# Performance work log

Hardware: AMD Instinct MI355X
Metric: run time of the kernel (lower is better)

The kernel has to match this reference:

```python
import jax, jax.numpy as jnp
import numpy as np

DIM, HEADS, DEPTH, SEQ, LOCAL_W = 1024, 16, 7, 2048, 64
HEAD_DIM = DIM // HEADS
SCALE = 1.0 / HEAD_DIM ** 0.5


def cantor_mask(S, depth, local_window):
    """Allowed (i,j): |i-j| within local window, OR |i-j| lies in the Cantor set
    under `depth` levels of ternary subdivision (no base-3 digit equals 1)."""
    idx = np.arange(S)
    d = np.abs(idx[:, None] - idx[None, :])
    x = d.copy()
    ok = np.ones_like(d, dtype=bool)
    for _ in range(depth):
        ok &= (x % 3) != 1
        x //= 3
    ok &= x == 0  # offset must be < 3**depth
    return jnp.asarray(ok | (d <= local_window))  # [S, S] bool


def setup_inputs() -> dict:
    key = jax.random.key(0)
    ks = jax.random.split(key, 8)
    B = 2
    s = 0.02
    return {
        "query": jax.random.normal(ks[0], (B, SEQ, DIM), jnp.float32),
        "key_value": jax.random.normal(ks[1], (B, SEQ, DIM), jnp.float32),
        "Wq": jax.random.normal(ks[2], (DIM, DIM), jnp.float32) * s,
        "bq": jnp.zeros((DIM,), jnp.float32),
        "Wkv": jax.random.normal(ks[3], (DIM, 2 * DIM), jnp.float32) * s,
        "bkv": jnp.zeros((2 * DIM,), jnp.float32),
        "Wo": jax.random.normal(ks[4], (DIM, DIM), jnp.float32) * s,
        "bo": jnp.zeros((DIM,), jnp.float32),
    }


def reference(query, key_value, Wq, bq, Wkv, bkv, Wo, bo):
    B, S, D = query.shape
    H, hd = HEADS, HEAD_DIM
    mask = cantor_mask(S, DEPTH, LOCAL_W)  # static [S, S] bool

    q = (query @ Wq + bq).reshape(B, S, H, hd).transpose(0, 2, 1, 3)  # [B,H,S,hd]
    kv = (key_value @ Wkv + bkv).reshape(B, S, 2, H, hd).transpose(2, 0, 3, 1, 4)
    k, v = kv[0], kv[1]  # [B,H,S,hd]

    scores = jnp.einsum("bhqd,bhkd->bhqk", q, k) * SCALE
    scores = jnp.where(mask, scores, jnp.finfo(scores.dtype).min)
    attn = jax.nn.softmax(scores, axis=-1)
    out = jnp.einsum("bhqk,bhkd->bhqd", attn, v)  # [B,H,S,hd]
    out = out.transpose(0, 2, 1, 3).reshape(B, S, D)
    return out @ Wo + bo
```

## Files before the change

kernel.cpp:

```cpp
#include <hip/hip_runtime.h>
#include <stdint.h>

typedef _Float16 half_t;
typedef __attribute__((ext_vector_type(8))) _Float16 half8;
typedef __attribute__((ext_vector_type(4))) _Float16 half4;
typedef __attribute__((ext_vector_type(4))) float floatx4;
typedef __attribute__((ext_vector_type(2))) uint32_t uint32x2;

#define SEQ 2048
#define NH 16
#define HD 64

#define MFMA16(a, b, c) __builtin_amdgcn_mfma_f32_16x16x16f16(a, b, c, 0, 0, 0)
#define MFMA32K(a, b, c) __builtin_amdgcn_mfma_f32_16x16x32_f16(a, b, c, 0, 0, 0)

#define QSCALE 0.1803368801111306f

__global__ __launch_bounds__(256) void prep(
    const float* __restrict__ query, const float* __restrict__ key_value,
    const float* __restrict__ Wq, const float* __restrict__ Wkv,
    const float* __restrict__ Wo, half_t* __restrict__ xq,
    half_t* __restrict__ xkv, half_t* __restrict__ wqT,
    half_t* __restrict__ wkvT, half_t* __restrict__ woT,
    uint8_t* __restrict__ tok, uint8_t* __restrict__ tok16,
    uint64_t* __restrict__ maskw) {
  int bx = blockIdx.x, tid = threadIdx.x;
  if (bx < 2048) {
    const float* s; half_t* d; int base;
    if (bx < 1024) { s = query; d = xq; base = bx * 4096; }
    else { s = key_value; d = xkv; base = (bx - 1024) * 4096; }
#pragma unroll
    for (int u = 0; u < 4; ++u) {
      int i = base + u * 1024 + tid * 4;
      floatx4 v = *(const floatx4*)(s + i);
      half4 h;
      h[0] = (half_t)v[0]; h[1] = (half_t)v[1];
      h[2] = (half_t)v[2]; h[3] = (half_t)v[3];
      *(half4*)(d + i) = h;
    }
    return;
  }
  if (bx < 4096) {
    __shared__ float tile[32][33];
    int tx = tid & 31, ty = tid >> 5;
    const int K = 1024;
#pragma unroll
    for (int u = 0; u < 2; ++u) {
      int t = (bx - 2048) * 2 + u;
      const float* W; half_t* Wt; int N, nt, kt;
      if (t < 1024) { W = Wq; Wt = wqT; N = 1024; nt = t & 31; kt = t >> 5; }
      else if (t < 3072) { int t2 = t - 1024; W = Wkv; Wt = wkvT; N = 2048; nt = t2 & 63; kt = t2 >> 6; }
      else { int t2 = t - 3072; W = Wo; Wt = woT; N = 1024; nt = t2 & 31; kt = t2 >> 5; }
      int n0 = nt * 32, k0 = kt * 32;
#pragma unroll
      for (int i = 0; i < 4; ++i)
        tile[ty + i * 8][tx] = W[(size_t)(k0 + ty + i * 8) * N + n0 + tx];
      __syncthreads();
#pragma unroll
      for (int i = 0; i < 4; ++i)
        Wt[(size_t)(n0 + ty + i * 8) * K + k0 + tx] = (half_t)tile[tx][ty + i * 8];
      __syncthreads();
    }
    return;
  }
  __shared__ uint8_t slut[2048];
  int ib = bx - 4096;
  for (int d = tid; d < 2048; d += 256) {
    int x = d;
    bool ok = true;
    for (int it = 0; it < 7; ++it) { ok &= ((x % 3) != 1); x /= 3; }
    ok &= (x == 0);
    slut[d] = (ok || d <= 64) ? 1 : 0;
  }
  __syncthreads();
  if (ib == 0) {
    if (tid < 64) {
      int delta = tid - 32;
      int lo = delta * 64 - 63, hi = delta * 64 + 63;
      uint8_t any = 0;
      for (int x = lo; x <= hi; ++x) {
        int a = x < 0 ? -x : x;
        if (a < 2048) any |= slut[a];
      }
      tok[tid] = any;
    }
    {
      int d16 = tid - 128;
      int ctr = d16 * 16;
      uint8_t any = 0;
      for (int x = ctr - 15; x <= ctr + 15; ++x) {
        int a = x < 0 ? -x : x;
        if (a < 2048) any |= slut[a];
      }
      tok16[tid] = any;
    }
  }
  int g = ib * 256 + tid;
  int tt = g - 2048;
  uint64_t w = 0;
  for (int jj = 0; jj < 64; ++jj) {
    int d = tt - jj; d = d < 0 ? -d : d;
    if (d < 2048 && slut[d]) w |= (1ull << jj);
  }
  maskw[g] = w;
}

__device__ __forceinline__ void cp16(half_t* lds, const half_t* g) {
  __builtin_amdgcn_global_load_lds(
      (const __attribute__((address_space(1))) uint32_t*)g,
      (__attribute__((address_space(3))) uint32_t*)lds, 16, 0, 0);
}

__global__ __launch_bounds__(256) void gemm_qkv(
    const half_t* __restrict__ xq, const half_t* __restrict__ xkv,
    const half_t* __restrict__ wqT, const half_t* __restrict__ wkvT,
    const float* __restrict__ bq, const float* __restrict__ bkv,
    half_t* __restrict__ qout, half_t* __restrict__ kout,
    half_t* __restrict__ vTout) {
  extern __shared__ char smemraw[];
  half_t* As = (half_t*)smemraw;
  half_t* Bs = As + 12288;
  const int K = 1024;
  bool isq = blockIdx.y < 8;
  const half_t* A = isq ? xq : xkv;
  const half_t* Bt = isq ? wqT : wkvT;
  const float* bias = isq ? bq : bkv;
  int n0 = (isq ? blockIdx.y : (blockIdx.y - 8)) * 128;
  int m0 = blockIdx.x * 128;

  int tid = threadIdx.x;
  int wave = tid >> 6, lane = tid & 63;
  int c = lane & 15, quad = lane >> 4;
  int wm = (wave >> 1) * 64, wn = (wave & 1) * 64;

  floatx4 acc[4][4] = {};
  int arow = tid >> 2;
  int akc = ((tid & 3) ^ (arow & 3)) * 8;
  int csw = c & 3;

#define QKV_ISSUE(kt2)                                                        \
  {                                                                           \
    int s_ = (kt2) % 3;                                                       \
    int k0_ = (kt2) * 32;                                                     \
    cp16(&As[s_ * 4096 + wave * 512], A + (size_t)(m0 + arow) * K + k0_ + akc);          \
    cp16(&As[s_ * 4096 + 2048 + wave * 512], A + (size_t)(m0 + 64 + arow) * K + k0_ + akc); \
    cp16(&Bs[s_ * 4096 + wave * 512], Bt + (size_t)(n0 + arow) * K + k0_ + akc);         \
    cp16(&Bs[s_ * 4096 + 2048 + wave * 512], Bt + (size_t)(n0 + 64 + arow) * K + k0_ + akc); \
  }

  QKV_ISSUE(0)
  QKV_ISSUE(1)

  for (int kt = 0; kt < 32; ++kt) {
    if (kt < 31) {
      asm volatile("s_waitcnt vmcnt(4)" ::: "memory");
    } else {
      asm volatile("s_waitcnt vmcnt(0)" ::: "memory");
    }
    __builtin_amdgcn_s_barrier();
    if (kt + 2 < 32) QKV_ISSUE(kt + 2)
    int b = kt % 3;
    half8 af[4], bf[4];
#pragma unroll
    for (int mt = 0; mt < 4; ++mt)
      af[mt] = *(const half8*)&As[b * 4096 + (wm + mt * 16 + c) * 32 + ((quad ^ csw) * 8)];
#pragma unroll
    for (int nt = 0; nt < 4; ++nt)
      bf[nt] = *(const half8*)&Bs[b * 4096 + (wn + nt * 16 + c) * 32 + ((quad ^ csw) * 8)];
#pragma unroll
    for (int mt = 0; mt < 4; ++mt)
#pragma unroll
      for (int nt = 0; nt < 4; ++nt)
        acc[mt][nt] = MFMA32K(af[mt], bf[nt], acc[mt][nt]);
  }
#undef QKV_ISSUE

  __syncthreads();
  half_t* ep = (half_t*)smemraw;
  int bb = m0 >> 11, sbase = m0 & 2047;
  bool isv = (!isq) && (n0 >= 1024);

  if (!isv) {
#pragma unroll
    for (int nt = 0; nt < 4; ++nt) {
      int nl = wn + nt * 16 + c;
      float bv = bias[n0 + nl];
#pragma unroll
      for (int mt = 0; mt < 4; ++mt)
#pragma unroll
        for (int r = 0; r < 4; ++r) {
          int ml = wm + mt * 16 + quad * 4 + r;
          float v = acc[mt][nt][r] + bv;
          if (isq) v *= QSCALE;
          ep[ml * 132 + nl] = (half_t)v;
        }
    }
    __syncthreads();
    half_t* outp = isq ? qout : kout;
#pragma unroll
    for (int rd = 0; rd < 8; ++rd) {
      int id = rd * 256 + tid;
      int ml = id >> 4, ch = id & 15;
      int ng = n0 + ch * 8;
      int h = ng >> 6, d0 = ng & 63;
      half8 v = *(const half8*)&ep[ml * 132 + ch * 8];
      *(half8*)(outp + ((size_t)(bb * 16 + h) * SEQ + sbase + ml) * 64 + d0) = v;
    }
  } else {
#pragma unroll
    for (int nt = 0; nt < 4; ++nt) {
      int nl = wn + nt * 16 + c;
      float bv = bias[n0 + nl];
#pragma unroll
      for (int mt = 0; mt < 4; ++mt) {
        int ml = wm + mt * 16 + quad * 4;
        half4 hv;
#pragma unroll
        for (int r = 0; r < 4; ++r) hv[r] = (half_t)(acc[mt][nt][r] + bv);
        *(half4*)&ep[nl * 136 + ml] = hv;
      }
    }
    __syncthreads();
#pragma unroll
    for (int rd = 0; rd < 8; ++rd) {
      int id = rd * 256 + tid;
      int nl = id >> 4, mc = id & 15;
      int ng = n0 + nl;
      int h = (ng >> 6) & 15, d = ng & 63;
      half8 v = *(const half8*)&ep[nl * 136 + mc * 8];
      *(half8*)(vTout + ((size_t)(bb * 16 + h) * 64 + d) * SEQ + sbase + mc * 8) = v;
    }
  }
}

__global__ __launch_bounds__(256) void gemm_out(
    const half_t* __restrict__ A, const half_t* __restrict__ Bt,
    const float* __restrict__ bias, float* __restrict__ outf) {
  __shared__ half_t As[3][128 * 32];
  __shared__ half_t Bs[3][64 * 32];
  const int K = 1024;
  int tid = threadIdx.x;
  int wave = tid >> 6, lane = tid & 63;
  int c = lane & 15, quad = lane >> 4;
  int wm = (wave >> 1) * 64, wn = (wave & 1) * 32;
  int m0 = blockIdx.x * 128, n0 = blockIdx.y * 64;

  floatx4 acc[4][2] = {};
  int arow = tid >> 2;
  int akc = ((tid & 3) ^ (arow & 3)) * 8;
  int csw = c & 3;

#define OUT_ISSUE(kt2)                                                        \
  {                                                                           \
    int s_ = (kt2) % 3;                                                       \
    int k0_ = (kt2) * 32;                                                     \
    cp16(&As[s_][wave * 512], A + (size_t)(m0 + arow) * K + k0_ + akc);       \
    cp16(&As[s_][2048 + wave * 512], A + (size_t)(m0 + 64 + arow) * K + k0_ + akc); \
    cp16(&Bs[s_][wave * 512], Bt + (size_t)(n0 + arow) * K + k0_ + akc);      \
  }

  OUT_ISSUE(0)
  OUT_ISSUE(1)

  for (int kt = 0; kt < 32; ++kt) {
    if (kt < 31) {
      asm volatile("s_waitcnt vmcnt(3)" ::: "memory");
    } else {
      asm volatile("s_waitcnt vmcnt(0)" ::: "memory");
    }
    __builtin_amdgcn_s_barrier();
    if (kt + 2 < 32) OUT_ISSUE(kt + 2)
    int b = kt % 3;
    half8 af[4], bf[2];
#pragma unroll
    for (int mt = 0; mt < 4; ++mt)
      af[mt] = *(const half8*)&As[b][(wm + mt * 16 + c) * 32 + ((quad ^ csw) * 8)];
#pragma unroll
    for (int nt = 0; nt < 2; ++nt)
      bf[nt] = *(const half8*)&Bs[b][(wn + nt * 16 + c) * 32 + ((quad ^ csw) * 8)];
#pragma unroll
    for (int mt = 0; mt < 4; ++mt)
#pragma unroll
      for (int nt = 0; nt < 2; ++nt)
        acc[mt][nt] = MFMA32K(af[mt], bf[nt], acc[mt][nt]);
  }
#undef OUT_ISSUE

#pragma unroll
  for (int nt = 0; nt < 2; ++nt) {
    int n = n0 + wn + nt * 16 + c;
    float bv = bias[n];
#pragma unroll
    for (int mt = 0; mt < 4; ++mt)
#pragma unroll
      for (int r = 0; r < 4; ++r) {
        int m = m0 + wm + mt * 16 + quad * 4 + r;
        outf[(size_t)m * 1024 + n] = acc[mt][nt][r] + bv;
      }
  }
}

__global__ __launch_bounds__(512) void attn_kernel(
    const half_t* __restrict__ qb, const half_t* __restrict__ kb,
    const half_t* __restrict__ vTg, half_t* __restrict__ ctx,
    const uint64_t* __restrict__ maskw, const uint8_t* __restrict__ tok,
    const uint8_t* __restrict__ tok16g) {
  __shared__ half_t kT[64 * 64];
  __shared__ half_t vT[64 * 64];
  __shared__ half_t ot[128 * 72];
  __shared__ int list[34];
  __shared__ uint8_t tok16s[256];
  __shared__ uint32_t mlut[16][2];

  int tid = threadIdx.x, wave = tid >> 6, lane = tid & 63;
  int c = lane & 15, q = lane >> 4;
  int id = blockIdx.x;
  int bh = (id & 7) * 4 + ((id >> 3) & 3);
  int it128 = id >> 5;
  int i0 = it128 << 7;
  const half_t* qbase = qb + (size_t)bh * SEQ * HD;
  const half_t* kg = kb + (size_t)bh * SEQ * HD;
  const half_t* vg = vTg + (size_t)bh * HD * SEQ;

  if (tid < 256) tok16s[tid] = tok16g[tid];
  if (tid >= 256 && tid < 272) {
    int t = tid - 256;
    mlut[t][0] = (t & 1 ? 0xFFFFu : 0u) | (t & 2 ? 0xFFFF0000u : 0u);
    mlut[t][1] = (t & 4 ? 0xFFFFu : 0u) | (t & 8 ? 0xFFFF0000u : 0u);
  }
  if (wave == 0) {
    int jt = lane;
    int base = i0 >> 6;
    bool act = (jt < 32) &&
               (tok[(jt - base) + 32] | tok[(jt - base - 1) + 32]);
    unsigned long long bal = __ballot(act);
    if (act) {
      int pre = __popcll(bal & ((1ull << jt) - 1));
      list[1 + pre] = jt << 6;
    }
    if (lane == 0) list[0] = __popcll(bal);
  }

  int i_row = i0 + wave * 16 + c;
  int it16 = (i0 >> 4) + wave;
  half8 qf0 = *(const half8*)(qbase + (size_t)i_row * 64 + q * 8);
  half8 qf1 = *(const half8*)(qbase + (size_t)i_row * 64 + 32 + q * 8);

  floatx4 oacc[4] = {};
  floatx4 lacc = {};
  half4 ones;
  ones[0] = (half_t)1.f; ones[1] = (half_t)1.f;
  ones[2] = (half_t)1.f; ones[3] = (half_t)1.f;

  int srow = tid >> 3;
  int sch = tid & 7;
  int ssw = srow & 7;

  __syncthreads();
  int nact = list[0];
  int j0 = list[1];

  half8 kr = *(const half8*)(kg + (size_t)(j0 + srow) * 64 + sch * 8);
  half8 vr = *(const half8*)(vg + (size_t)srow * SEQ + j0 + sch * 8);
  uint64_t wcur = maskw[(i_row - j0) + 2048];

  for (int ti = 0; ti < nact; ++ti) {
    int bidx = (j0 >> 4) - it16 + 128;
    __syncthreads();
    *(half8*)&kT[srow * 64 + ((sch ^ ssw) * 8)] = kr;
    *(half8*)&vT[srow * 64 + ((sch ^ ssw) * 8)] = vr;
    int j0n = (ti + 1 < nact) ? list[2 + ti] : j0;
    __syncthreads();

    uint64_t wnext = wcur;
    if (ti + 1 < nact) {
      kr = *(const half8*)(kg + (size_t)(j0n + srow) * 64 + sch * 8);
      vr = *(const half8*)(vg + (size_t)srow * SEQ + j0n + sch * 8);
      wnext = maskw[(i_row - j0n) + 2048];
    }

    uint32_t wlo = (uint32_t)(wcur >> (4 * q));
    uint32_t whi = (uint32_t)(wcur >> (32 + 4 * q));
    uint32x2 mm[4];
#pragma unroll
    for (int jt = 0; jt < 4; ++jt) {
      uint32_t ww = (jt < 2) ? wlo : whi;
      uint32_t nib = (ww >> (16 * (jt & 1))) & 15u;
      mm[jt] = *(const uint32x2*)&mlut[nib][0];
    }
#pragma unroll
    for (int jt = 0; jt < 4; ++jt) {
      if (!tok16s[bidx + jt]) continue;
      int row = jt * 16 + c;
      int sw = c & 7;
      half8 a0 = *(const half8*)&kT[row * 64 + ((q ^ sw) * 8)];
      half8 a1 = *(const half8*)&kT[row * 64 + (((4 + q) ^ sw) * 8)];
      floatx4 t = {};
      t = MFMA32K(a0, qf0, t);
      t = MFMA32K(a1, qf1, t);
      float p0 = __builtin_exp2f(t[0]);
      float p1 = __builtin_exp2f(t[1]);
      float p2 = __builtin_exp2f(t[2]);
      float p3 = __builtin_exp2f(t[3]);
      auto lo = __builtin_amdgcn_cvt_pkrtz(p0, p1);
      auto hi = __builtin_amdgcn_cvt_pkrtz(p2, p3);
      union { uint32_t u[2]; half4 h4; } pu;
      pu.u[0] = __builtin_bit_cast(uint32_t, lo) & mm[jt][0];
      pu.u[1] = __builtin_bit_cast(uint32_t, hi) & mm[jt][1];
      half4 pb = pu.h4;
      lacc = MFMA16(ones, pb, lacc);
#pragma unroll
      for (int mt = 0; mt < 4; ++mt) {
        int drow = mt * 16 + c;
        int ch = 2 * jt + (q >> 1);
        half4 a = *(const half4*)&vT[drow * 64 + ((ch ^ sw) * 8) + (q & 1) * 4];
        oacc[mt] = MFMA16(a, pb, oacc[mt]);
      }
    }
    wcur = wnext;
    j0 = j0n;
  }

  float inv_l = 1.0f / lacc[0];
#pragma unroll
  for (int mt = 0; mt < 4; ++mt)
#pragma unroll
    for (int r = 0; r < 4; ++r)
      ot[(wave * 16 + c) * 72 + mt * 16 + 4 * q + r] = (half_t)(oacc[mt][r] * inv_l);
  __syncthreads();
  {
    int row = tid >> 2, chq = tid & 3;
    int b = bh >> 4, h = bh & 15;
    size_t base = (((size_t)(b * SEQ + i0 + row) * NH) + h) * 64 + chq * 16;
    half8 v0 = *(const half8*)&ot[row * 72 + chq * 16];
    half8 v1 = *(const half8*)&ot[row * 72 + chq * 16 + 8];
    *(half8*)(ctx + base) = v0;
    *(half8*)(ctx + base + 8) = v1;
  }
}

extern "C" void kernel_launch(void* const* d_in, const int* in_sizes, int n_in,
                              void* d_out, int out_size, void* d_ws, size_t ws_size,
                              hipStream_t stream) {
  const float* query = (const float*)d_in[0];
  const float* key_value = (const float*)d_in[1];
  const float* Wq = (const float*)d_in[2];
  const float* bq = (const float*)d_in[3];
  const float* Wkv = (const float*)d_in[4];
  const float* bkv = (const float*)d_in[5];
  const float* Wo = (const float*)d_in[6];
  const float* bo = (const float*)d_in[7];

  char* ws = (char*)d_ws;
  uint8_t* tok = (uint8_t*)ws;
  uint8_t* tok16 = (uint8_t*)(ws + 1024);
  uint64_t* maskw = (uint64_t*)(ws + 4096);
  const size_t MB = 1ull << 20;
  half_t* xq = (half_t*)(ws + 1 * MB);
  half_t* xkv = (half_t*)(ws + 9 * MB);
  half_t* wqT = (half_t*)(ws + 17 * MB);
  half_t* wkvT = (half_t*)(ws + 19 * MB);
  half_t* woT = (half_t*)(ws + 23 * MB);
  half_t* qbuf = (half_t*)(ws + 25 * MB);
  half_t* kbuf = (half_t*)(ws + 33 * MB);
  half_t* vTg = (half_t*)(ws + 41 * MB);
  half_t* ctx = xq;

  hipLaunchKernelGGL(prep, dim3(4112), dim3(256), 0, stream,
                     query, key_value, Wq, Wkv, Wo, xq, xkv, wqT, wkvT, woT,
                     tok, tok16, maskw);
  hipLaunchKernelGGL(gemm_qkv, dim3(32, 24), dim3(256), 49152, stream,
                     xq, xkv, wqT, wkvT, bq, bkv, qbuf, kbuf, vTg);
  hipLaunchKernelGGL(attn_kernel, dim3(512), dim3(512), 0, stream,
                     qbuf, kbuf, vTg, ctx, maskw, tok, tok16);
  hipLaunchKernelGGL(gemm_out, dim3(32, 16), dim3(256), 0, stream,
                     ctx, woT, bo, (float*)d_out);
}
```

Before: 210.6 us.

## Enlarge QKV GEMM to 256x256 tiles with 8 waves and phased pipelining

Rewrites the QKV projection GEMM to use 256x256 output tiles per 512-thread block with K-step 64 and double-buffered LDS of 128KB. The main loop is split into four quadrant phases, each overlapping the async global-to-LDS loads for the next K tile with MFMA work, using sched_barrier and setprio. The aim is to raise arithmetic intensity and hide load latency better than the earlier 128x128 triple-buffered loop. The trade-off is only 192 blocks on the grid with one block per CU, so fill of the wave-level work may drop, and register pressure rises from the larger accumulator set.

New measurement: 220.0 us. 1.04x slower.

```diff
diff --git a/kernel.cpp b/kernel.cpp
--- a/kernel.cpp
+++ b/kernel.cpp
@@ -111,7 +111,53 @@
       (__attribute__((address_space(3))) uint32_t*)lds, 16, 0, 0);
 }
 
-__global__ __launch_bounds__(256) void gemm_qkv(
+#define VMC(n) asm volatile("s_waitcnt vmcnt(" #n ")" ::: "memory")
+
+#define STG_A(kt2, mh)                                                        \
+  {                                                                           \
+    half_t* d_ = &As[(((kt2) & 1) * 2 + (mh)) * 8192 + wave * 512];           \
+    const half_t* s_ = A + (size_t)(m0 + (mh) * 128 + r1) * K + (kt2) * 64 + hsw; \
+    cp16(d_, s_);                                                             \
+    cp16(d_ + 4096, s_ + (size_t)64 * K);                                     \
+  }
+#define STG_B(kt2, nh)                                                        \
+  {                                                                           \
+    half_t* d_ = &Bs[(((kt2) & 1) * 2 + (nh)) * 8192 + wave * 512];           \
+    const half_t* s_ = Bt + (size_t)(n0 + (nh) * 128 + r1) * K + (kt2) * 64 + hsw; \
+    cp16(d_, s_);                                                             \
+    cp16(d_ + 4096, s_ + (size_t)64 * K);                                     \
+  }
+
+#define PHASE(KB, MQ, NQ, ...)                                                \
+  do {                                                                        \
+    __builtin_amdgcn_s_barrier();                                             \
+    __builtin_amdgcn_sched_barrier(0);                                        \
+    const half_t* Ab = &As[((KB) * 2 + (MQ)) * 8192];                         \
+    const half_t* Bb = &Bs[((KB) * 2 + (NQ)) * 8192];                         \
+    half8 af[4][2], bf[2][2];                                                 \
+    _Pragma("unroll") for (int i_ = 0; i_ < 4; ++i_) {                        \
+      int rl_ = mw * 64 + i_ * 16 + c;                                        \
+      af[i_][0] = *(const half8*)&Ab[rl_ * 64 + ((quad * 8) ^ rsw)];          \
+      af[i_][1] = *(const half8*)&Ab[rl_ * 64 + ((32 + quad * 8) ^ rsw)];     \
+    }                                                                         \
+    _Pragma("unroll") for (int j_ = 0; j_ < 2; ++j_) {                        \
+      int cl_ = nw * 32 + j_ * 16 + c;                                        \
+      bf[j_][0] = *(const half8*)&Bb[cl_ * 64 + ((quad * 8) ^ rsw)];          \
+      bf[j_][1] = *(const half8*)&Bb[cl_ * 64 + ((32 + quad * 8) ^ rsw)];     \
+    }                                                                         \
+    __VA_ARGS__;                                                              \
+    __builtin_amdgcn_sched_barrier(0);                                        \
+    __builtin_amdgcn_s_barrier();                                             \
+    __builtin_amdgcn_s_setprio(1);                                            \
+    _Pragma("unroll") for (int i_ = 0; i_ < 4; ++i_)                          \
+      _Pragma("unroll") for (int j_ = 0; j_ < 2; ++j_) {                      \
+        acc[MQ][NQ][i_][j_] = MFMA32K(af[i_][0], bf[j_][0], acc[MQ][NQ][i_][j_]); \
+        acc[MQ][NQ][i_][j_] = MFMA32K(af[i_][1], bf[j_][1], acc[MQ][NQ][i_][j_]); \
+      }                                                                       \
+    __builtin_amdgcn_s_setprio(0);                                            \
+  } while (0)
+
+__global__ __launch_bounds__(512, 1) void gemm_qkv(
     const half_t* __restrict__ xq, const half_t* __restrict__ xkv,
     const half_t* __restrict__ wqT, const half_t* __restrict__ wkvT,
     const float* __restrict__ bq, const float* __restrict__ bkv,
@@ -119,61 +165,43 @@
     half_t* __restrict__ vTout) {
   extern __shared__ char smemraw[];
   half_t* As = (half_t*)smemraw;
-  half_t* Bs = As + 12288;
-  const int K = 1024;
-  bool isq = blockIdx.y < 8;
+  half_t* Bs = As + 32768;
+  const int K = 1024, NT = 16;
+  bool isq = blockIdx.y < 4;
   const half_t* A = isq ? xq : xkv;
   const half_t* Bt = isq ? wqT : wkvT;
   const float* bias = isq ? bq : bkv;
-  int n0 = (isq ? blockIdx.y : (blockIdx.y - 8)) * 128;
-  int m0 = blockIdx.x * 128;
+  int n0 = (isq ? blockIdx.y : (blockIdx.y - 4)) * 256;
+  int m0 = blockIdx.x * 256;
 
   int tid = threadIdx.x;
   int wave = tid >> 6, lane = tid & 63;
   int c = lane & 15, quad = lane >> 4;
-  int wm = (wave >> 1) * 64, wn = (wave & 1) * 64;
-
-  floatx4 acc[4][4] = {};
-  int arow = tid >> 2;
-  int akc = ((tid & 3) ^ (arow & 3)) * 8;
-  int csw = c & 3;
-
-#define QKV_ISSUE(kt2)                                                        \
-  {                                                                           \
-    int s_ = (kt2) % 3;                                                       \
-    int k0_ = (kt2) * 32;                                                     \
-    cp16(&As[s_ * 4096 + wave * 512], A + (size_t)(m0 + arow) * K + k0_ + akc);          \
-    cp16(&As[s_ * 4096 + 2048 + wave * 512], A + (size_t)(m0 + 64 + arow) * K + k0_ + akc); \
-    cp16(&Bs[s_ * 4096 + wave * 512], Bt + (size_t)(n0 + arow) * K + k0_ + akc);         \
-    cp16(&Bs[s_ * 4096 + 2048 + wave * 512], Bt + (size_t)(n0 + 64 + arow) * K + k0_ + akc); \
-  }
-
-  QKV_ISSUE(0)
-  QKV_ISSUE(1)
-
-  for (int kt = 0; kt < 32; ++kt) {
-    if (kt < 31) {
-      asm volatile("s_waitcnt vmcnt(4)" ::: "memory");
-    } else {
-      asm volatile("s_waitcnt vmcnt(0)" ::: "memory");
-    }
-    __builtin_amdgcn_s_barrier();
-    if (kt + 2 < 32) QKV_ISSUE(kt + 2)
-    int b = kt % 3;
-    half8 af[4], bf[4];
-#pragma unroll
-    for (int mt = 0; mt < 4; ++mt)
-      af[mt] = *(const half8*)&As[b * 4096 + (wm + mt * 16 + c) * 32 + ((quad ^ csw) * 8)];
-#pragma unroll
-    for (int nt = 0; nt < 4; ++nt)
-      bf[nt] = *(const half8*)&Bs[b * 4096 + (wn + nt * 16 + c) * 32 + ((quad ^ csw) * 8)];
-#pragma unroll
-    for (int mt = 0; mt < 4; ++mt)
-#pragma unroll
-      for (int nt = 0; nt < 4; ++nt)
-        acc[mt][nt] = MFMA32K(af[mt], bf[nt], acc[mt][nt]);
-  }
-#undef QKV_ISSUE
+  int mw = wave >> 2, nw = wave & 3;
+
+  floatx4 acc[2][2][4][2] = {};
+
+  int r1 = tid >> 3;
+  int hh = (tid & 7) * 8;
+  int hsw = hh ^ (((r1 >> 2) & 1) << 4);
+  int rsw = ((c >> 2) & 1) << 4;
+
+  STG_A(0, 0); STG_B(0, 0); STG_B(0, 1); STG_A(0, 1);
+
+  for (int kt = 0; kt + 1 < NT; ++kt) {
+    int kb = kt & 1, kn = kt + 1;
+    VMC(4); PHASE(kb, 0, 0, STG_A(kn, 0));
+    VMC(4); PHASE(kb, 0, 1, STG_B(kn, 0));
+    VMC(4); PHASE(kb, 1, 0, STG_B(kn, 1));
+            PHASE(kb, 1, 1, STG_A(kn, 1));
+  }
+  {
+    int kb = (NT - 1) & 1;
+    VMC(4); PHASE(kb, 0, 0, (void)0);
+    VMC(2); PHASE(kb, 0, 1, (void)0);
+    VMC(0); PHASE(kb, 1, 0, (void)0);
+            PHASE(kb, 1, 1, (void)0);
+  }
 
   __syncthreads();
   half_t* ep = (half_t*)smemraw;
@@ -181,57 +209,71 @@
   bool isv = (!isq) && (n0 >= 1024);
 
   if (!isv) {
-#pragma unroll
-    for (int nt = 0; nt < 4; ++nt) {
-      int nl = wn + nt * 16 + c;
-      float bv = bias[n0 + nl];
-#pragma unroll
-      for (int mt = 0; mt < 4; ++mt)
-#pragma unroll
-        for (int r = 0; r < 4; ++r) {
-          int ml = wm + mt * 16 + quad * 4 + r;
-          float v = acc[mt][nt][r] + bv;
-          if (isq) v *= QSCALE;
-          ep[ml * 132 + nl] = (half_t)v;
-        }
-    }
-    __syncthreads();
     half_t* outp = isq ? qout : kout;
 #pragma unroll
-    for (int rd = 0; rd < 8; ++rd) {
-      int id = rd * 256 + tid;
-      int ml = id >> 4, ch = id & 15;
-      int ng = n0 + ch * 8;
-      int h = ng >> 6, d0 = ng & 63;
-      half8 v = *(const half8*)&ep[ml * 132 + ch * 8];
-      *(half8*)(outp + ((size_t)(bb * 16 + h) * SEQ + sbase + ml) * 64 + d0) = v;
+    for (int nq = 0; nq < 2; ++nq) {
+      if (nq) __syncthreads();
+#pragma unroll
+      for (int mq = 0; mq < 2; ++mq)
+#pragma unroll
+        for (int i = 0; i < 4; ++i)
+#pragma unroll
+          for (int j = 0; j < 2; ++j) {
+            int row = mq * 128 + mw * 64 + i * 16 + quad * 4;
+            int cl = nw * 32 + j * 16 + c;
+            float bv = bias[n0 + nq * 128 + cl];
+#pragma unroll
+            for (int r = 0; r < 4; ++r) {
+              float v = acc[mq][nq][i][j][r] + bv;
+              if (isq) v *= QSCALE;
+              ep[(row + r) * 132 + cl] = (half_t)v;
+            }
+          }
+      __syncthreads();
+#pragma unroll
+      for (int rd = 0; rd < 8; ++rd) {
+        int id = rd * 512 + tid;
+        int ml = id >> 4, ch = id & 15;
+        int ng = n0 + nq * 128 + ch * 8;
+        int h = ng >> 6, d0 = ng & 63;
+        half8 v = *(const half8*)&ep[ml * 132 + ch * 8];
+        *(half8*)(outp + ((size_t)(bb * 16 + h) * SEQ + sbase + ml) * 64 + d0) = v;
+      }
     }
   } else {
 #pragma unroll
-    for (int nt = 0; nt < 4; ++nt) {
-      int nl = wn + nt * 16 + c;
-      float bv = bias[n0 + nl];
-#pragma unroll
-      for (int mt = 0; mt < 4; ++mt) {
-        int ml = wm + mt * 16 + quad * 4;
-        half4 hv;
-#pragma unroll
-        for (int r = 0; r < 4; ++r) hv[r] = (half_t)(acc[mt][nt][r] + bv);
-        *(half4*)&ep[nl * 136 + ml] = hv;
+    for (int nq = 0; nq < 2; ++nq) {
+      if (nq) __syncthreads();
+#pragma unroll
+      for (int mq = 0; mq < 2; ++mq)
+#pragma unroll
+        for (int i = 0; i < 4; ++i)
+#pragma unroll
+          for (int j = 0; j < 2; ++j) {
+            int row = mq * 128 + mw * 64 + i * 16 + quad * 4;
+            int cl = nw * 32 + j * 16 + c;
+            float bv = bias[n0 + nq * 128 + cl];
+            half4 hv;
+#pragma unroll
+            for (int r = 0; r < 4; ++r) hv[r] = (half_t)(acc[mq][nq][i][j][r] + bv);
+            *(half4*)&ep[cl * 264 + row] = hv;
+          }
+      __syncthreads();
+#pragma unroll
+      for (int rd = 0; rd < 8; ++rd) {
+        int id = rd * 512 + tid;
+        int dl = id >> 5, mc = id & 31;
+        int ng = n0 + nq * 128 + dl;
+        int h = (ng >> 6) & 15, d = ng & 63;
+        half8 v = *(const half8*)&ep[dl * 264 + mc * 8];
+        *(half8*)(vTout + ((size_t)(bb * 16 + h) * 64 + d) * SEQ + sbase + mc * 8) = v;
       }
     }
-    __syncthreads();
-#pragma unroll
-    for (int rd = 0; rd < 8; ++rd) {
-      int id = rd * 256 + tid;
-      int nl = id >> 4, mc = id & 15;
-      int ng = n0 + nl;
-      int h = (ng >> 6) & 15, d = ng & 63;
-      half8 v = *(const half8*)&ep[nl * 136 + mc * 8];
-      *(half8*)(vTout + ((size_t)(bb * 16 + h) * 64 + d) * SEQ + sbase + mc * 8) = v;
-    }
   }
 }
+#undef PHASE
+#undef STG_A
+#undef STG_B
 
 __global__ __launch_bounds__(256) void gemm_out(
     const half_t* __restrict__ A, const half_t* __restrict__ Bt,
@@ -469,7 +511,7 @@
   hipLaunchKernelGGL(prep, dim3(4112), dim3(256), 0, stream,
                      query, key_value, Wq, Wkv, Wo, xq, xkv, wqT, wkvT, woT,
                      tok, tok16, maskw);
-  hipLaunchKernelGGL(gemm_qkv, dim3(32, 24), dim3(256), 49152, stream,
+  hipLaunchKernelGGL(gemm_qkv, dim3(16, 12), dim3(512), 131072, stream,
                      xq, xkv, wqT, wkvT, bq, bkv, qbuf, kbuf, vTg);
   hipLaunchKernelGGL(attn_kernel, dim3(512), dim3(512), 0, stream,
                      qbuf, kbuf, vTg, ctx, maskw, tok, tok16);
```
